# Performance work log

Hardware: AMD Instinct MI355X
Metric: run time of the kernel (lower is better)

The kernel has to match this reference:

```python
import jax, jax.numpy as jnp
import numpy as np

N_NODES = 50000
N_EDGES = 800000
NFEAT = 128
NHID = 128
NCLASS = 10
NUM_GRAPHS = 512


def setup_inputs() -> dict:
    key = jax.random.key(0)
    ks = jax.random.split(key, 8)
    node_feat = jax.random.normal(ks[0], (N_NODES, NFEAT), dtype=jnp.float32)
    W1 = jax.random.normal(ks[1], (NFEAT, NHID), dtype=jnp.float32) * (1.0 / np.sqrt(NFEAT))
    W2 = jax.random.normal(ks[2], (NHID, NHID), dtype=jnp.float32) * (1.0 / np.sqrt(NHID))
    mlp_w = jax.random.normal(ks[3], (NHID, NCLASS), dtype=jnp.float32) * (1.0 / np.sqrt(NHID))
    mlp_b = jnp.zeros((NCLASS,), dtype=jnp.float32)
    edge_src = jax.random.randint(ks[4], (N_EDGES,), 0, N_NODES, dtype=jnp.int32)
    edge_dst = jax.random.randint(ks[5], (N_EDGES,), 0, N_NODES, dtype=jnp.int32)
    graph_ids = jnp.sort(jax.random.randint(ks[6], (N_NODES,), 0, NUM_GRAPHS, dtype=jnp.int32))
    return {"node_feat": node_feat, "W1": W1, "W2": W2, "mlp_w": mlp_w,
            "mlp_b": mlp_b, "edge_src": edge_src, "edge_dst": edge_dst,
            "graph_ids": graph_ids}


def reference(node_feat, W1, W2, mlp_w, mlp_b, edge_src, edge_dst, graph_ids):
    # node_degs: in-degree + 1 (self loop), as used by GraphConvolution's normalization
    ones_e = jnp.ones((N_EDGES,), dtype=node_feat.dtype)
    deg = jax.ops.segment_sum(ones_e, edge_dst, num_segments=N_NODES) + 1.0  # [N]

    def gconv(x, W):
        h = x @ W                                                     # [N, H]
        msg = jax.ops.segment_sum(h[edge_src], edge_dst, num_segments=N_NODES)
        return (h + msg) / deg[:, None]                               # mean over self + neighbors

    x = jax.nn.relu(gconv(node_feat, W1))
    x = gconv(x, W2)                                                  # [N, NHID]

    # per-graph mean readout (the Python loop over graph_sizes == segment mean)
    counts = jax.ops.segment_sum(jnp.ones((N_NODES,), x.dtype), graph_ids,
                                 num_segments=NUM_GRAPHS)             # [G]
    gsum = jax.ops.segment_sum(x, graph_ids, num_segments=NUM_GRAPHS)  # [G, NHID]
    gmean = gsum / jnp.maximum(counts, 1.0)[:, None]

    logits = gmean @ mlp_w + mlp_b                                    # [G, NCLASS]
    return jax.nn.log_softmax(logits, axis=1)
```

## Files before the change

kernel.cpp:

```cpp
#include <hip/hip_runtime.h>

#define N_NODES 50000
#define N_EDGES 800000
#define NFEAT 128
#define NHID 128
#define NCLASS 10
#define NUM_GRAPHS 512
#define GEMM_BLOCKS 391
#define SLOT 64
#define NBUK 391
#define ECAP 512
#define CPAD 32

typedef __attribute__((ext_vector_type(8))) short bf16x8;
typedef __attribute__((ext_vector_type(4))) float f32x4;

__device__ inline ushort f2bf(float f) {
  union { float f; uint u; } c; c.f = f;
  return (ushort)((c.u + 0x7fffu + ((c.u >> 16) & 1u)) >> 16);
}
__device__ inline float bf2f_lo(uint u) { union { uint u; float f; } c; c.u = u << 16; return c.f; }
__device__ inline float bf2f_hi(uint u) { union { uint u; float f; } c; c.u = u & 0xffff0000u; return c.f; }
__device__ inline float bf2f_s(ushort h) { union { uint u; float f; } c; c.u = ((uint)h) << 16; return c.f; }

template <bool XFP32>
__device__ inline void gemm_body(const void* __restrict__ Xv,
                                 const ushort* __restrict__ Wp,
                                 ushort* __restrict__ Y,
                                 ushort* xs, ushort* wsh,
                                 int base, int tid) {
  const int rem = N_NODES - base;
  for (int i = tid; i < 2048; i += 512)
    ((uint4*)wsh)[i] = ((const uint4*)Wp)[i];

  for (int g = tid; g < 2048; g += 512) {
    int row = g >> 4;
    int k0 = (g & 15) << 3;
    int wt = row >> 4, ks = k0 >> 5;
    int lane = (row & 15) + (((k0 >> 3) & 3) << 4);
    uint4 v;
    if (row < rem) {
      if (XFP32) {
        const float* s = (const float*)Xv + (size_t)(base + row) * 128 + k0;
        float4 p0 = ((const float4*)s)[0];
        float4 p1 = ((const float4*)s)[1];
        v.x = (uint)f2bf(p0.x) | ((uint)f2bf(p0.y) << 16);
        v.y = (uint)f2bf(p0.z) | ((uint)f2bf(p0.w) << 16);
        v.z = (uint)f2bf(p1.x) | ((uint)f2bf(p1.y) << 16);
        v.w = (uint)f2bf(p1.z) | ((uint)f2bf(p1.w) << 16);
      } else {
        v = *(const uint4*)((const ushort*)Xv + (size_t)(base + row) * 128 + k0);
      }
    } else {
      v.x = 0; v.y = 0; v.z = 0; v.w = 0;
    }
    *(uint4*)&xs[((((wt << 2) + ks) << 6) + lane) << 3] = v;
  }
  __syncthreads();

  const int wave = tid >> 6, lane = tid & 63;
  f32x4 acc[8];
#pragma unroll
  for (int i = 0; i < 8; ++i) acc[i] = f32x4{0.f, 0.f, 0.f, 0.f};
  bf16x8 a[4];
#pragma unroll
  for (int ks = 0; ks < 4; ++ks)
    a[ks] = *(const bf16x8*)&xs[((((wave << 2) + ks) << 6) + lane) << 3];
#pragma unroll
  for (int ks = 0; ks < 4; ++ks) {
#pragma unroll
    for (int nt = 0; nt < 8; ++nt) {
      bf16x8 b = *(const bf16x8*)&wsh[((((nt << 2) + ks) << 6) + lane) << 3];
      acc[nt] = __builtin_amdgcn_mfma_f32_16x16x32_bf16(a[ks], b, acc[nt], 0, 0, 0);
    }
  }
  const int r0 = base + wave * 16 + ((lane >> 4) << 2);
  const int c0 = lane & 15;
#pragma unroll
  for (int nt = 0; nt < 8; ++nt)
#pragma unroll
    for (int r = 0; r < 4; ++r) {
      int row = r0 + r;
      if (row < N_NODES)
        Y[(size_t)row * 128 + (nt << 4) + c0] = f2bf(acc[nt][r]);
    }
}

__global__ __launch_bounds__(512) void k_gemm1(const float* __restrict__ X,
                                               const ushort* __restrict__ Wp,
                                               ushort* __restrict__ Y) {
  __shared__ ushort xs[8 * 4 * 64 * 8];
  __shared__ ushort wsh[32 * 64 * 8];
  gemm_body<true>(X, Wp, Y, xs, wsh, blockIdx.x * 128, threadIdx.x);
}

__global__ __launch_bounds__(512) void k_gemm2(const ushort* __restrict__ X,
                                               const ushort* __restrict__ Wp,
                                               ushort* __restrict__ Y) {
  __shared__ ushort xs[8 * 4 * 64 * 8];
  __shared__ ushort wsh[32 * 64 * 8];
  gemm_body<false>(X, Wp, Y, xs, wsh, blockIdx.x * 128, threadIdx.x);
}

__global__ __launch_bounds__(256) void k_wpack(const float* __restrict__ W1,
                                               const float* __restrict__ W2,
                                               ushort* __restrict__ wp1,
                                               ushort* __restrict__ wp2) {
  int idx = blockIdx.x * 256 + threadIdx.x;
  const float* W = (idx < 16384) ? W1 : W2;
  ushort* op = (idx < 16384) ? wp1 : wp2;
  int j = idx & 16383;
  int lane = (j >> 3) & 63;
  int e = j & 7;
  int frag = j >> 9;
  int nt = frag >> 2, ks = frag & 3;
  int c = nt * 16 + (lane & 15);
  int k = ks * 32 + (lane >> 4) * 8 + e;
  op[j] = f2bf(W[k * 128 + c]);
}

__global__ __launch_bounds__(256) void k_scat(const int* __restrict__ esrc,
                                              const int* __restrict__ edst,
                                              int* __restrict__ cnt8,
                                              uint* __restrict__ ebuf) {
  uint xcc;
  asm volatile("s_getreg_b32 %0, hwreg(HW_REG_XCC_ID)" : "=s"(xcc));
  const int x = (int)(xcc & 7);
  for (int e = blockIdx.x * 256 + threadIdx.x; e < N_EDGES; e += gridDim.x * 256) {
    int d = edst[e];
    int bk = d >> 7;
    int dloc = d & 127;
    int p = atomicAdd(&cnt8[((bk << 3) + x) * CPAD], 1);
    if (p < ECAP)
      ebuf[(((size_t)bk << 3) + x) * ECAP + p] = (uint)esrc[e] | ((uint)dloc << 16);
  }
}

__global__ __launch_bounds__(256) void k_csr(const uint* __restrict__ ebuf,
                                             const int* __restrict__ cnt8,
                                             ushort* __restrict__ csr16,
                                             int* __restrict__ cnt) {
  __shared__ ushort csr_l[4096];
  __shared__ int cntL[128], off[128], cur[128];
  __shared__ int len8[8];
  const int b = blockIdx.x, tid = threadIdx.x;
  const int n0 = b << 7;
  const int nmax = min(128, N_NODES - n0);
  if (tid < 8) len8[tid] = min(cnt8[((b << 3) + tid) * CPAD], ECAP);
  for (int i = tid; i < 128; i += 256) { cntL[i] = 0; cur[i] = 0; }
  __syncthreads();
#pragma unroll
  for (int x = 0; x < 8; ++x) {
    const uint* s = ebuf + (((size_t)b << 3) + x) * ECAP;
    for (int i = tid; i < len8[x]; i += 256)
      atomicAdd(&cntL[s[i] >> 16], 1);
  }
  __syncthreads();
  if (tid == 0) {
    int o = 0;
    for (int n = 0; n < 128; ++n) { off[n] = o; o += min(cntL[n], SLOT); }
  }
  __syncthreads();
#pragma unroll
  for (int x = 0; x < 8; ++x) {
    const uint* s = ebuf + (((size_t)b << 3) + x) * ECAP;
    for (int i = tid; i < len8[x]; i += 256) {
      uint u = s[i];
      int dl = u >> 16;
      int p = atomicAdd(&cur[dl], 1);
      if (p < SLOT) csr_l[off[dl] + p] = (ushort)(u & 0xffffu);
    }
  }
  __syncthreads();
  for (int n = tid; n < nmax; n += 256) cnt[n0 + n] = min(cntL[n], SLOT);
  uint* outp = (uint*)csr16 + ((size_t)n0 << 5);
  const int tot = nmax << 5;
  for (int j = tid; j < tot; j += 256) {
    int n = j >> 5, k = (j & 31) << 1;
    int c = min(cntL[n], SLOT);
    uint lo = (k < c) ? (uint)csr_l[off[n] + k] : 0u;
    uint hi = (k + 1 < c) ? (uint)csr_l[off[n] + k + 1] : 0u;
    outp[((size_t)n << 5) + (j & 31)] = lo | (hi << 16);
  }
}

__device__ inline void unpack_add(uint4 u, float4& a0, float4& a1) {
  a0.x += bf2f_lo(u.x); a0.y += bf2f_hi(u.x);
  a0.z += bf2f_lo(u.y); a0.w += bf2f_hi(u.y);
  a1.x += bf2f_lo(u.z); a1.y += bf2f_hi(u.z);
  a1.z += bf2f_lo(u.w); a1.w += bf2f_hi(u.w);
}

__device__ inline void gather_sum(const uint4* __restrict__ Hv,
                                  const ushort* __restrict__ nb,
                                  int deg, int q, float4& a0, float4& a1) {
  int e = 0;
  for (; e + 8 <= deg; e += 8) {
    uint4 iv = *(const uint4*)(nb + e);
    uint4 u0 = Hv[(size_t)(iv.x & 0xffffu) * 16 + q];
    uint4 u1 = Hv[(size_t)(iv.x >> 16) * 16 + q];
    uint4 u2 = Hv[(size_t)(iv.y & 0xffffu) * 16 + q];
    uint4 u3 = Hv[(size_t)(iv.y >> 16) * 16 + q];
    uint4 u4 = Hv[(size_t)(iv.z & 0xffffu) * 16 + q];
    uint4 u5 = Hv[(size_t)(iv.z >> 16) * 16 + q];
    uint4 u6 = Hv[(size_t)(iv.w & 0xffffu) * 16 + q];
    uint4 u7 = Hv[(size_t)(iv.w >> 16) * 16 + q];
    unpack_add(u0, a0, a1); unpack_add(u1, a0, a1);
    unpack_add(u2, a0, a1); unpack_add(u3, a0, a1);
    unpack_add(u4, a0, a1); unpack_add(u5, a0, a1);
    unpack_add(u6, a0, a1); unpack_add(u7, a0, a1);
  }
  if (e + 4 <= deg) {
    uint2 iv = *(const uint2*)(nb + e);
    uint4 u0 = Hv[(size_t)(iv.x & 0xffffu) * 16 + q];
    uint4 u1 = Hv[(size_t)(iv.x >> 16) * 16 + q];
    uint4 u2 = Hv[(size_t)(iv.y & 0xffffu) * 16 + q];
    uint4 u3 = Hv[(size_t)(iv.y >> 16) * 16 + q];
    unpack_add(u0, a0, a1); unpack_add(u1, a0, a1);
    unpack_add(u2, a0, a1); unpack_add(u3, a0, a1);
    e += 4;
  }
  for (; e < deg; ++e) {
    uint4 u = Hv[(size_t)nb[e] * 16 + q];
    unpack_add(u, a0, a1);
  }
}

__global__ __launch_bounds__(256) void k_agg1(const ushort* __restrict__ H,
                                              const ushort* __restrict__ csr16,
                                              const int* __restrict__ cnt,
                                              ushort* __restrict__ Out) {
  const int q = threadIdx.x & 15;
  const int node = blockIdx.x * 16 + (threadIdx.x >> 4);
  const int deg = min(cnt[node], SLOT);
  const ushort* nb = csr16 + (size_t)node * SLOT;
  const uint4* __restrict__ Hv = (const uint4*)H;
  float4 a0 = {0.f, 0.f, 0.f, 0.f}, a1 = {0.f, 0.f, 0.f, 0.f};
  gather_sum(Hv, nb, deg, q, a0, a1);
  uint4 uh = Hv[(size_t)node * 16 + q];
  float inv = 1.0f / (float)(deg + 1);
  float v0 = fmaxf((bf2f_lo(uh.x) + a0.x) * inv, 0.f);
  float v1 = fmaxf((bf2f_hi(uh.x) + a0.y) * inv, 0.f);
  float v2 = fmaxf((bf2f_lo(uh.y) + a0.z) * inv, 0.f);
  float v3 = fmaxf((bf2f_hi(uh.y) + a0.w) * inv, 0.f);
  float v4 = fmaxf((bf2f_lo(uh.z) + a1.x) * inv, 0.f);
  float v5 = fmaxf((bf2f_hi(uh.z) + a1.y) * inv, 0.f);
  float v6 = fmaxf((bf2f_lo(uh.w) + a1.z) * inv, 0.f);
  float v7 = fmaxf((bf2f_hi(uh.w) + a1.w) * inv, 0.f);
  uint4 ov;
  ov.x = (uint)f2bf(v0) | ((uint)f2bf(v1) << 16);
  ov.y = (uint)f2bf(v2) | ((uint)f2bf(v3) << 16);
  ov.z = (uint)f2bf(v4) | ((uint)f2bf(v5) << 16);
  ov.w = (uint)f2bf(v6) | ((uint)f2bf(v7) << 16);
  ((uint4*)Out)[(size_t)node * 16 + q] = ov;
}

__global__ __launch_bounds__(256) void k_agg_ro(const ushort* __restrict__ H,
                                                const ushort* __restrict__ csr16,
                                                const int* __restrict__ cnt,
                                                const int* __restrict__ gid,
                                                float* __restrict__ gsum,
                                                float* __restrict__ gcnt) {
  __shared__ float rows[16][128];
  __shared__ int gids[16];
  const int q = threadIdx.x & 15;
  const int slot = threadIdx.x >> 4;
  const int node = blockIdx.x * 16 + slot;
  const int deg = min(cnt[node], SLOT);
  const ushort* nb = csr16 + (size_t)node * SLOT;
  const uint4* __restrict__ Hv = (const uint4*)H;
  float4 a0 = {0.f, 0.f, 0.f, 0.f}, a1 = {0.f, 0.f, 0.f, 0.f};
  gather_sum(Hv, nb, deg, q, a0, a1);
  uint4 uh = Hv[(size_t)node * 16 + q];
  float inv = 1.0f / (float)(deg + 1);
  float4 r0, r1;
  r0.x = bf2f_s(f2bf((bf2f_lo(uh.x) + a0.x) * inv));
  r0.y = bf2f_s(f2bf((bf2f_hi(uh.x) + a0.y) * inv));
  r0.z = bf2f_s(f2bf((bf2f_lo(uh.y) + a0.z) * inv));
  r0.w = bf2f_s(f2bf((bf2f_hi(uh.y) + a0.w) * inv));
  r1.x = bf2f_s(f2bf((bf2f_lo(uh.z) + a1.x) * inv));
  r1.y = bf2f_s(f2bf((bf2f_hi(uh.z) + a1.y) * inv));
  r1.z = bf2f_s(f2bf((bf2f_lo(uh.w) + a1.z) * inv));
  r1.w = bf2f_s(f2bf((bf2f_hi(uh.w) + a1.w) * inv));
  *(float4*)&rows[slot][q * 8] = r0;
  *(float4*)&rows[slot][q * 8 + 4] = r1;
  if (q == 0) gids[slot] = gid[node];
  __syncthreads();
  const int t = threadIdx.x;
  if (t < 128) {
    float acc = rows[0][t];
    int g = gids[0];
#pragma unroll
    for (int r = 1; r < 16; ++r) {
      int gr = gids[r];
      if (gr != g) {
        atomicAdd(&gsum[g * 128 + t], acc);
        acc = 0.f;
        g = gr;
      }
      acc += rows[r][t];
    }
    atomicAdd(&gsum[g * 128 + t], acc);
  } else if (t == 128) {
    float c = 1.f;
    int g = gids[0];
#pragma unroll
    for (int r = 1; r < 16; ++r) {
      int gr = gids[r];
      if (gr != g) {
        atomicAdd(&gcnt[g], c);
        c = 0.f;
        g = gr;
      }
      c += 1.f;
    }
    atomicAdd(&gcnt[g], c);
  }
}

__global__ __launch_bounds__(128) void k_mlp(const float* __restrict__ gsum,
                                             const float* __restrict__ gcnt,
                                             const float* __restrict__ Wm,
                                             const float* __restrict__ bm,
                                             float* __restrict__ out) {
  __shared__ float m[128];
  __shared__ float lg[NCLASS];
  const int g = blockIdx.x;
  const int t = threadIdx.x;
  float cnt = fmaxf(gcnt[g], 1.0f);
  m[t] = gsum[g * 128 + t] / cnt;
  __syncthreads();
  if (t < NCLASS) {
    float s = bm[t];
#pragma unroll
    for (int k = 0; k < 128; ++k) s += m[k] * Wm[k * NCLASS + t];
    lg[t] = s;
  }
  __syncthreads();
  if (t < NCLASS) {
    float mx = lg[0];
#pragma unroll
    for (int i = 1; i < NCLASS; ++i) mx = fmaxf(mx, lg[i]);
    float sum = 0.f;
#pragma unroll
    for (int i = 0; i < NCLASS; ++i) sum += expf(lg[i] - mx);
    out[g * NCLASS + t] = lg[t] - mx - logf(sum);
  }
}

extern "C" void kernel_launch(void* const* d_in, const int* in_sizes, int n_in,
                              void* d_out, int out_size, void* d_ws, size_t ws_size,
                              hipStream_t stream) {
  const float* feat = (const float*)d_in[0];
  const float* W1   = (const float*)d_in[1];
  const float* W2   = (const float*)d_in[2];
  const float* Wm   = (const float*)d_in[3];
  const float* bm   = (const float*)d_in[4];
  const int* esrc   = (const int*)d_in[5];
  const int* edst   = (const int*)d_in[6];
  const int* gid    = (const int*)d_in[7];
  float* out = (float*)d_out;

  int* cnt8     = (int*)d_ws;
  int* cnt      = cnt8 + NBUK * 8 * CPAD;
  uint* ebuf    = (uint*)(cnt + 50048);
  ushort* csr16 = (ushort*)(ebuf + (size_t)NBUK * 8 * ECAP);
  ushort* wp1   = csr16 + (size_t)50048 * SLOT;
  ushort* wp2   = wp1 + 16384;
  ushort* bufA  = wp2 + 16384;
  ushort* bufB  = bufA + (size_t)N_NODES * NHID;
  float* gsum   = (float*)(bufB + (size_t)N_NODES * NHID);
  float* gcnt   = gsum + NUM_GRAPHS * NHID;

  hipMemsetAsync(cnt8, 0, (size_t)NBUK * 8 * CPAD * sizeof(int), stream);
  hipMemsetAsync(gsum, 0, (size_t)(NUM_GRAPHS * NHID + 512) * sizeof(float), stream);

  k_wpack<<<128, 256, 0, stream>>>(W1, W2, wp1, wp2);
  k_scat<<<1024, 256, 0, stream>>>(esrc, edst, cnt8, ebuf);
  k_csr<<<NBUK, 256, 0, stream>>>(ebuf, cnt8, csr16, cnt);

  k_gemm1<<<GEMM_BLOCKS, 512, 0, stream>>>(feat, wp1, bufA);
  k_agg1<<<N_NODES / 16, 256, 0, stream>>>(bufA, csr16, cnt, bufB);
  k_gemm2<<<GEMM_BLOCKS, 512, 0, stream>>>(bufB, wp2, bufA);
  k_agg_ro<<<N_NODES / 16, 256, 0, stream>>>(bufA, csr16, cnt, gid, gsum, gcnt);

  k_mlp<<<NUM_GRAPHS, 128, 0, stream>>>(gsum, gcnt, Wm, bm, out);
}
```

Measured before the change: 230.0 us.

## Reassociate GCN layers: aggregate before W1, move W2 after graph readout

Uses linearity to reorder the work. Layer 1 now aggregates the raw features (converted to bf16 by a new kernel) and then applies W1 with a fused ReLU. Layer 2 aggregates the post-ReLU activations directly, and W2 is applied per graph after the mean readout inside the MLP kernel, so the second node-level GEMM is gone. The cost is an extra full-feature conversion pass and a small per-graph 128x128 matvec. Rounding also changes, since intermediate bf16 roundings are removed in the readout path.

```diff
diff --git a/kernel.cpp b/kernel.cpp
--- a/kernel.cpp
+++ b/kernel.cpp
@@ -21,10 +21,9 @@
 }
 __device__ inline float bf2f_lo(uint u) { union { uint u; float f; } c; c.u = u << 16; return c.f; }
 __device__ inline float bf2f_hi(uint u) { union { uint u; float f; } c; c.u = u & 0xffff0000u; return c.f; }
-__device__ inline float bf2f_s(ushort h) { union { uint u; float f; } c; c.u = ((uint)h) << 16; return c.f; }
-
-template <bool XFP32>
-__device__ inline void gemm_body(const void* __restrict__ Xv,
+
+template <bool RELU>
+__device__ inline void gemm_body(const ushort* __restrict__ Xv,
                                  const ushort* __restrict__ Wp,
                                  ushort* __restrict__ Y,
                                  ushort* xs, ushort* wsh,
@@ -40,17 +39,7 @@
     int lane = (row & 15) + (((k0 >> 3) & 3) << 4);
     uint4 v;
     if (row < rem) {
-      if (XFP32) {
-        const float* s = (const float*)Xv + (size_t)(base + row) * 128 + k0;
-        float4 p0 = ((const float4*)s)[0];
-        float4 p1 = ((const float4*)s)[1];
-        v.x = (uint)f2bf(p0.x) | ((uint)f2bf(p0.y) << 16);
-        v.y = (uint)f2bf(p0.z) | ((uint)f2bf(p0.w) << 16);
-        v.z = (uint)f2bf(p1.x) | ((uint)f2bf(p1.y) << 16);
-        v.w = (uint)f2bf(p1.z) | ((uint)f2bf(p1.w) << 16);
-      } else {
-        v = *(const uint4*)((const ushort*)Xv + (size_t)(base + row) * 128 + k0);
-      }
+      v = *(const uint4*)(Xv + (size_t)(base + row) * 128 + k0);
     } else {
       v.x = 0; v.y = 0; v.z = 0; v.w = 0;
     }
@@ -81,12 +70,15 @@
 #pragma unroll
     for (int r = 0; r < 4; ++r) {
       int row = r0 + r;
-      if (row < N_NODES)
-        Y[(size_t)row * 128 + (nt << 4) + c0] = f2bf(acc[nt][r]);
-    }
-}
-
-__global__ __launch_bounds__(512) void k_gemm1(const float* __restrict__ X,
+      if (row < N_NODES) {
+        float v = acc[nt][r];
+        if (RELU) v = fmaxf(v, 0.f);
+        Y[(size_t)row * 128 + (nt << 4) + c0] = f2bf(v);
+      }
+    }
+}
+
+__global__ __launch_bounds__(512) void k_gemm1(const ushort* __restrict__ X,
                                                const ushort* __restrict__ Wp,
                                                ushort* __restrict__ Y) {
   __shared__ ushort xs[8 * 4 * 64 * 8];
@@ -94,22 +86,9 @@
   gemm_body<true>(X, Wp, Y, xs, wsh, blockIdx.x * 128, threadIdx.x);
 }
 
-__global__ __launch_bounds__(512) void k_gemm2(const ushort* __restrict__ X,
-                                               const ushort* __restrict__ Wp,
-                                               ushort* __restrict__ Y) {
-  __shared__ ushort xs[8 * 4 * 64 * 8];
-  __shared__ ushort wsh[32 * 64 * 8];
-  gemm_body<false>(X, Wp, Y, xs, wsh, blockIdx.x * 128, threadIdx.x);
-}
-
-__global__ __launch_bounds__(256) void k_wpack(const float* __restrict__ W1,
-                                               const float* __restrict__ W2,
-                                               ushort* __restrict__ wp1,
-                                               ushort* __restrict__ wp2) {
-  int idx = blockIdx.x * 256 + threadIdx.x;
-  const float* W = (idx < 16384) ? W1 : W2;
-  ushort* op = (idx < 16384) ? wp1 : wp2;
-  int j = idx & 16383;
+__global__ __launch_bounds__(256) void k_wpack(const float* __restrict__ W,
+                                               ushort* __restrict__ op) {
+  int j = blockIdx.x * 256 + threadIdx.x;
   int lane = (j >> 3) & 63;
   int e = j & 7;
   int frag = j >> 9;
@@ -117,6 +96,16 @@
   int c = nt * 16 + (lane & 15);
   int k = ks * 32 + (lane >> 4) * 8 + e;
   op[j] = f2bf(W[k * 128 + c]);
+}
+
+__global__ __launch_bounds__(256) void k_cvt(const float* __restrict__ f,
+                                             ushort* __restrict__ o) {
+  int i = blockIdx.x * 256 + threadIdx.x;
+  float4 v = ((const float4*)f)[i];
+  uint2 p;
+  p.x = (uint)f2bf(v.x) | ((uint)f2bf(v.y) << 16);
+  p.y = (uint)f2bf(v.z) | ((uint)f2bf(v.w) << 16);
+  ((uint2*)o)[i] = p;
 }
 
 __global__ __launch_bounds__(256) void k_scat(const int* __restrict__ esrc,
@@ -226,7 +215,7 @@
   }
 }
 
-__global__ __launch_bounds__(256) void k_agg1(const ushort* __restrict__ H,
+__global__ __launch_bounds__(256) void k_agg0(const ushort* __restrict__ H,
                                               const ushort* __restrict__ csr16,
                                               const int* __restrict__ cnt,
                                               ushort* __restrict__ Out) {
@@ -239,14 +228,14 @@
   gather_sum(Hv, nb, deg, q, a0, a1);
   uint4 uh = Hv[(size_t)node * 16 + q];
   float inv = 1.0f / (float)(deg + 1);
-  float v0 = fmaxf((bf2f_lo(uh.x) + a0.x) * inv, 0.f);
-  float v1 = fmaxf((bf2f_hi(uh.x) + a0.y) * inv, 0.f);
-  float v2 = fmaxf((bf2f_lo(uh.y) + a0.z) * inv, 0.f);
-  float v3 = fmaxf((bf2f_hi(uh.y) + a0.w) * inv, 0.f);
-  float v4 = fmaxf((bf2f_lo(uh.z) + a1.x) * inv, 0.f);
-  float v5 = fmaxf((bf2f_hi(uh.z) + a1.y) * inv, 0.f);
-  float v6 = fmaxf((bf2f_lo(uh.w) + a1.z) * inv, 0.f);
-  float v7 = fmaxf((bf2f_hi(uh.w) + a1.w) * inv, 0.f);
+  float v0 = (bf2f_lo(uh.x) + a0.x) * inv;
+  float v1 = (bf2f_hi(uh.x) + a0.y) * inv;
+  float v2 = (bf2f_lo(uh.y) + a0.z) * inv;
+  float v3 = (bf2f_hi(uh.y) + a0.w) * inv;
+  float v4 = (bf2f_lo(uh.z) + a1.x) * inv;
+  float v5 = (bf2f_hi(uh.z) + a1.y) * inv;
+  float v6 = (bf2f_lo(uh.w) + a1.z) * inv;
+  float v7 = (bf2f_hi(uh.w) + a1.w) * inv;
   uint4 ov;
   ov.x = (uint)f2bf(v0) | ((uint)f2bf(v1) << 16);
   ov.y = (uint)f2bf(v2) | ((uint)f2bf(v3) << 16);
@@ -274,14 +263,14 @@
   uint4 uh = Hv[(size_t)node * 16 + q];
   float inv = 1.0f / (float)(deg + 1);
   float4 r0, r1;
-  r0.x = bf2f_s(f2bf((bf2f_lo(uh.x) + a0.x) * inv));
-  r0.y = bf2f_s(f2bf((bf2f_hi(uh.x) + a0.y) * inv));
-  r0.z = bf2f_s(f2bf((bf2f_lo(uh.y) + a0.z) * inv));
-  r0.w = bf2f_s(f2bf((bf2f_hi(uh.y) + a0.w) * inv));
-  r1.x = bf2f_s(f2bf((bf2f_lo(uh.z) + a1.x) * inv));
-  r1.y = bf2f_s(f2bf((bf2f_hi(uh.z) + a1.y) * inv));
-  r1.z = bf2f_s(f2bf((bf2f_lo(uh.w) + a1.z) * inv));
-  r1.w = bf2f_s(f2bf((bf2f_hi(uh.w) + a1.w) * inv));
+  r0.x = (bf2f_lo(uh.x) + a0.x) * inv;
+  r0.y = (bf2f_hi(uh.x) + a0.y) * inv;
+  r0.z = (bf2f_lo(uh.y) + a0.z) * inv;
+  r0.w = (bf2f_hi(uh.y) + a0.w) * inv;
+  r1.x = (bf2f_lo(uh.z) + a1.x) * inv;
+  r1.y = (bf2f_hi(uh.z) + a1.y) * inv;
+  r1.z = (bf2f_lo(uh.w) + a1.z) * inv;
+  r1.w = (bf2f_hi(uh.w) + a1.w) * inv;
   *(float4*)&rows[slot][q * 8] = r0;
   *(float4*)&rows[slot][q * 8 + 4] = r1;
   if (q == 0) gids[slot] = gid[node];
@@ -318,23 +307,30 @@
   }
 }
 
-__global__ __launch_bounds__(128) void k_mlp(const float* __restrict__ gsum,
-                                             const float* __restrict__ gcnt,
-                                             const float* __restrict__ Wm,
-                                             const float* __restrict__ bm,
-                                             float* __restrict__ out) {
+__global__ __launch_bounds__(128) void k_mlp2(const float* __restrict__ gsum,
+                                              const float* __restrict__ gcnt,
+                                              const float* __restrict__ W2,
+                                              const float* __restrict__ Wm,
+                                              const float* __restrict__ bm,
+                                              float* __restrict__ out) {
   __shared__ float m[128];
+  __shared__ float h[128];
   __shared__ float lg[NCLASS];
   const int g = blockIdx.x;
   const int t = threadIdx.x;
-  float cnt = fmaxf(gcnt[g], 1.0f);
-  m[t] = gsum[g * 128 + t] / cnt;
+  float c = fmaxf(gcnt[g], 1.0f);
+  m[t] = gsum[g * 128 + t] / c;
+  __syncthreads();
+  float s = 0.f;
+#pragma unroll
+  for (int k = 0; k < 128; ++k) s += m[k] * W2[k * 128 + t];
+  h[t] = s;
   __syncthreads();
   if (t < NCLASS) {
-    float s = bm[t];
-#pragma unroll
-    for (int k = 0; k < 128; ++k) s += m[k] * Wm[k * NCLASS + t];
-    lg[t] = s;
+    float l = bm[t];
+#pragma unroll
+    for (int k = 0; k < 128; ++k) l += h[k] * Wm[k * NCLASS + t];
+    lg[t] = l;
   }
   __syncthreads();
   if (t < NCLASS) {
@@ -366,8 +362,7 @@
   uint* ebuf    = (uint*)(cnt + 50048);
   ushort* csr16 = (ushort*)(ebuf + (size_t)NBUK * 8 * ECAP);
   ushort* wp1   = csr16 + (size_t)50048 * SLOT;
-  ushort* wp2   = wp1 + 16384;
-  ushort* bufA  = wp2 + 16384;
+  ushort* bufA  = wp1 + 16384;
   ushort* bufB  = bufA + (size_t)N_NODES * NHID;
   float* gsum   = (float*)(bufB + (size_t)N_NODES * NHID);
   float* gcnt   = gsum + NUM_GRAPHS * NHID;
@@ -375,14 +370,13 @@
   hipMemsetAsync(cnt8, 0, (size_t)NBUK * 8 * CPAD * sizeof(int), stream);
   hipMemsetAsync(gsum, 0, (size_t)(NUM_GRAPHS * NHID + 512) * sizeof(float), stream);
 
-  k_wpack<<<128, 256, 0, stream>>>(W1, W2, wp1, wp2);
+  k_wpack<<<64, 256, 0, stream>>>(W1, wp1);
+  k_cvt<<<(N_NODES * NHID / 4 + 255) / 256, 256, 0, stream>>>(feat, bufA);
   k_scat<<<1024, 256, 0, stream>>>(esrc, edst, cnt8, ebuf);
   k_csr<<<NBUK, 256, 0, stream>>>(ebuf, cnt8, csr16, cnt);
 
-  k_gemm1<<<GEMM_BLOCKS, 512, 0, stream>>>(feat, wp1, bufA);
-  k_agg1<<<N_NODES / 16, 256, 0, stream>>>(bufA, csr16, cnt, bufB);
-  k_gemm2<<<GEMM_BLOCKS, 512, 0, stream>>>(bufB, wp2, bufA);
+  k_agg0<<<N_NODES / 16, 256, 0, stream>>>(bufA, csr16, cnt, bufB);
+  k_gemm1<<<GEMM_BLOCKS, 512, 0, stream>>>(bufB, wp1, bufA);
   k_agg_ro<<<N_NODES / 16, 256, 0, stream>>>(bufA, csr16, cnt, gid, gsum, gcnt);
-
-  k_mlp<<<NUM_GRAPHS, 128, 0, stream>>>(gsum, gcnt, Wm, bm, out);
-}
+  k_mlp2<<<NUM_GRAPHS, 128, 0, stream>>>(gsum, gcnt, W2, Wm, bm, out);
+}
```

After: 225.6 us. No clear change (-1.9%).
